# Kernel optimization log

Measured on AMD Instinct MI355X. Metric: run time of the kernel, lower is better.

## Reference

```python
import jax, jax.numpy as jnp
import numpy as np

B, S, D, H = 4, 2048, 1024, 16
HD = D // H
THETA = 10000.0


def rope(x, pos, theta=THETA):
    # x: [..., seq, d], pos: broadcastable to [..., seq]
    d = x.shape[-1]
    half = d // 2
    inv_freq = 1.0 / (theta ** (jnp.arange(half, dtype=jnp.float32) * 2.0 / d))  # [half]
    ang = pos[..., None].astype(jnp.float32) * inv_freq  # [..., seq, half]
    cos, sin = jnp.cos(ang), jnp.sin(ang)
    x1, x2 = x[..., 0::2], x[..., 1::2]
    r1 = x1 * cos - x2 * sin
    r2 = x1 * sin + x2 * cos
    return jnp.stack([r1, r2], axis=-1).reshape(x.shape).astype(x.dtype)


def setup_inputs() -> dict:
    key = jax.random.key(0)
    ks = jax.random.split(key, 5)
    x = jax.random.normal(ks[0], (B, S, D), dtype=jnp.float32)
    token_positions = jnp.tile(jnp.arange(S, dtype=jnp.int64 if jax.config.jax_enable_x64 else jnp.int32), (B, 1))
    scale = 0.02
    Wq = jax.random.normal(ks[1], (D, D), dtype=jnp.float32) * scale
    Wk = jax.random.normal(ks[2], (D, D), dtype=jnp.float32) * scale
    Wv = jax.random.normal(ks[3], (D, D), dtype=jnp.float32) * scale
    Wo = jax.random.normal(ks[4], (D, D), dtype=jnp.float32) * scale
    return {"x": x, "token_positions": token_positions, "Wq": Wq, "Wk": Wk, "Wv": Wv, "Wo": Wo}


def reference(x, token_positions, Wq, Wk, Wv, Wo):
    b, s, d = x.shape
    # QKV projections (torch Linear: x @ W.T), split heads -> [b, h, s, hd]
    def proj(W):
        y = jnp.einsum('bsd,ed->bse', x, W)
        return y.reshape(b, s, H, HD).transpose(0, 2, 1, 3)
    Q, K, V = proj(Wq), proj(Wk), proj(Wv)
    # token_positions [..., seq] -> [..., 1, seq] to broadcast over heads
    pos = token_positions[:, None, :]  # [b, 1, s]
    Q = rope(Q, pos)
    K = rope(K, pos)
    # causal mask and scaled dot-product attention
    idx = jnp.arange(s)
    causal = idx[:, None] >= idx[None, :]  # [s, s], query >= key
    scores = jnp.einsum('bhqd,bhkd->bhqk', Q, K) / jnp.sqrt(jnp.float32(HD))
    scores = jnp.where(causal, scores, -jnp.inf)
    weights = jax.nn.softmax(scores, axis=-1)
    o = jnp.einsum('bhqk,bhkd->bhqd', weights, V)
    o = o.transpose(0, 2, 1, 3).reshape(b, s, d)  # merge heads
    return jnp.einsum('bsd,ed->bse', o, Wo)
```

## Files before the change

### kernel.cpp

```cpp
#include <hip/hip_runtime.h>

#define S_LEN 2048
#define NH 16
#define HDIM 64
#define DMODEL 1024

typedef __attribute__((ext_vector_type(8))) short bf16x8;
typedef __attribute__((ext_vector_type(4))) float f32x4;

__device__ __forceinline__ short f2bf(float f) {
    union { float f; unsigned u; } x; x.f = f;
    unsigned r = x.u + 0x7fffu + ((x.u >> 16) & 1u);
    return (short)(r >> 16);
}

#define GLDS(g, l) __builtin_amdgcn_global_load_lds( \
    (__attribute__((address_space(1))) void*)(g),    \
    (__attribute__((address_space(3))) void*)(l), 16, 0, 0)

#define QSCALE 0.18033688011112042f
#define FREQ_L 0.41524101186109327f

__global__ __launch_bounds__(256) void prep(const float* __restrict__ x,
                                            const float* __restrict__ wq,
                                            const float* __restrict__ wk,
                                            const float* __restrict__ wv,
                                            const float* __restrict__ wo,
                                            const int* __restrict__ tp,
                                            short* __restrict__ xb,
                                            short* __restrict__ wqb,
                                            short* __restrict__ wkb,
                                            short* __restrict__ wvb,
                                            short* __restrict__ wob,
                                            float2* __restrict__ tab) {
    int bid = blockIdx.x;
    if (bid < 8192) {
        int i = bid * 256 + threadIdx.x;
        float4 v = ((const float4*)x)[i];
        short4 o;
        o.x = f2bf(v.x); o.y = f2bf(v.y); o.z = f2bf(v.z); o.w = f2bf(v.w);
        ((short4*)xb)[i] = o;
    } else if (bid < 12288) {
        int sel = (bid - 8192) >> 10;
        const float* in = sel == 0 ? wq : sel == 1 ? wk : sel == 2 ? wv : wo;
        short* out = sel == 0 ? wqb : sel == 1 ? wkb : sel == 2 ? wvb : wob;
        int i = ((bid - 8192) & 1023) * 256 + threadIdx.x;
        float4 v = ((const float4*)in)[i];
        short4 o;
        o.x = f2bf(v.x); o.y = f2bf(v.y); o.z = f2bf(v.z); o.w = f2bf(v.w);
        ((short4*)out)[i] = o;
    } else {
        int idx = (bid - 12288) * 256 + threadIdx.x;
        int b = idx >> 16, s = (idx >> 5) & 2047, i = idx & 31;
        float p = (float)tp[(b << 11) + s];
        float freq = exp2f(-(float)i * FREQ_L);
        float sn, cs;
        sincosf(p * freq, &sn, &cs);
        tab[idx] = make_float2(cs, sn);
    }
}

__global__ __launch_bounds__(512) void gemm_qkv(const short* __restrict__ A,
                                                const short* __restrict__ Bq,
                                                const short* __restrict__ Bk,
                                                const short* __restrict__ Bv,
                                                const float2* __restrict__ tab,
                                                short* __restrict__ Qo,
                                                short* __restrict__ Ko,
                                                short* __restrict__ Vo) {
    constexpr int K = 1024;
    __shared__ __align__(16) short smem[3 * 24576];

    const int sel = blockIdx.x >> 3;
    const int bn = blockIdx.x & 7;
    const int bm = blockIdx.y;
    const short* Bm = sel == 0 ? Bq : sel == 1 ? Bk : Bv;
    short* Cb = sel == 0 ? Qo : sel == 1 ? Ko : Vo;

    const int tid = threadIdx.x;
    const int lane = tid & 63;
    const int w = tid >> 6;
    const int wm = w >> 1;
    const int wn = w & 1;
    const int quad = lane >> 4, l16 = lane & 15;
    const int l7 = l16 & 7;

    int aoff[4], boff[2];
#pragma unroll
    for (int i = 0; i < 4; i++) {
        int Lc = i * 512 + tid;
        int row = Lc >> 3;
        int cc = (Lc & 7) ^ (row & 7);
        aoff[i] = (bm * 256 + row) * K + cc * 8;
    }
#pragma unroll
    for (int i = 0; i < 2; i++) {
        int Lc = i * 512 + tid;
        int row = Lc >> 3;
        int cc = (Lc & 7) ^ (row & 7);
        boff[i] = (bn * 128 + row) * K + cc * 8;
    }

    auto stage = [&](int h, int slot) {
        char* sbase = (char*)smem + slot * 49152;
        const int kh = h * 64;
#pragma unroll
        for (int i = 0; i < 4; i++)
            GLDS(A + aoff[i] + kh, sbase + i * 8192 + w * 1024);
#pragma unroll
        for (int i = 0; i < 2; i++)
            GLDS(Bm + boff[i] + kh, sbase + 32768 + i * 8192 + w * 1024);
    };

    f32x4 acc[4][4] = {};

    auto compute = [&](int slot) {
        const short* sA = smem + slot * 24576;
        const short* sB = sA + 16384;
#pragma unroll
        for (int kc = 0; kc < 2; kc++) {
            const int c = ((kc * 4 + quad) ^ l7) * 8;
            bf16x8 af[4], bfm[4];
#pragma unroll
            for (int mi = 0; mi < 4; mi++)
                af[mi] = *(const bf16x8*)&sA[(wm * 64 + mi * 16 + l16) * 64 + c];
#pragma unroll
            for (int ni = 0; ni < 4; ni++)
                bfm[ni] = *(const bf16x8*)&sB[(wn * 64 + ni * 16 + l16) * 64 + c];
            __builtin_amdgcn_s_setprio(1);
#pragma unroll
            for (int mi = 0; mi < 4; mi++)
#pragma unroll
                for (int ni = 0; ni < 4; ni++)
                    acc[mi][ni] = __builtin_amdgcn_mfma_f32_16x16x32_bf16(af[mi], bfm[ni],
                                                                          acc[mi][ni], 0, 0, 0);
            __builtin_amdgcn_s_setprio(0);
        }
    };

    stage(0, 0); stage(1, 1);

    auto step = [&](int h, int sc, int ss) {
        asm volatile("s_waitcnt vmcnt(6)" ::: "memory");
        __builtin_amdgcn_s_barrier();
        __builtin_amdgcn_sched_barrier(0);
        stage(h + 2, ss);
        compute(sc);
    };

    for (int h = 0; h < 12; h += 3) {
        step(h + 0, 0, 2);
        step(h + 1, 1, 0);
        step(h + 2, 2, 1);
    }
    step(12, 0, 2);
    step(13, 1, 0);
    asm volatile("s_waitcnt vmcnt(6)" ::: "memory");
    __builtin_amdgcn_s_barrier();
    __builtin_amdgcn_sched_barrier(0);
    compute(2);
    asm volatile("s_waitcnt vmcnt(0)" ::: "memory");
    __builtin_amdgcn_s_barrier();
    __builtin_amdgcn_sched_barrier(0);
    compute(0);

    const int gm0 = bm * 256 + wm * 64;
    const int gn0 = bn * 128 + wn * 64;

    if (sel == 2) {
        short* T = smem;
        __syncthreads();
#pragma unroll
        for (int mi = 0; mi < 4; mi++) {
            int lmb = wm * 64 + mi * 16 + quad * 4;
#pragma unroll
            for (int ni = 0; ni < 4; ni++) {
                int ln = wn * 64 + ni * 16 + l16;
                short4 pk;
                pk.x = f2bf(acc[mi][ni][0]);
                pk.y = f2bf(acc[mi][ni][1]);
                pk.z = f2bf(acc[mi][ni][2]);
                pk.w = f2bf(acc[mi][ni][3]);
                *(short4*)&T[ln * 256 + (lmb ^ ((ln & 31) << 3))] = pk;
            }
        }
        __syncthreads();
        const int row = tid >> 2, qt = tid & 3;
        const int grow = bn * 128 + row;
        const int gb = bm >> 3;
        const int gs0 = (bm & 7) * 256;
        short* dst = Cb + (((size_t)(gb * NH + (grow >> 6)) * HDIM + (grow & 63)) * S_LEN
                           + gs0 + qt * 64);
#pragma unroll
        for (int j = 0; j < 8; j++) {
            bf16x8 v = *(const bf16x8*)&T[row * 256 +
                        ((qt * 64 + j * 8) ^ ((row & 31) << 3))];
            *(bf16x8*)(dst + j * 8) = v;
        }
    } else {
        const float qs = (sel == 0) ? QSCALE : 1.0f;
#pragma unroll
        for (int mi = 0; mi < 4; mi++)
#pragma unroll
            for (int r = 0; r < 4; r++) {
                int gm = gm0 + mi * 16 + quad * 4 + r;
                const float2* trow = tab + (gm << 5);
                int b = gm >> 11, s = gm & 2047;
#pragma unroll
                for (int ni = 0; ni < 4; ni++) {
                    float2 cs = trow[ni * 8 + (l16 >> 1)];
                    float v = acc[mi][ni][r];
                    float prt = __shfl_xor(v, 1, 64);
                    float val = (l16 & 1) ? (prt * cs.y + v * cs.x)
                                          : (v * cs.x - prt * cs.y);
                    int gn = gn0 + ni * 16 + l16;
                    int h = gn >> 6, hd = gn & 63;
                    Cb[((b * NH + h) * S_LEN + s) * HDIM + hd] = f2bf(val * qs);
                }
            }
    }
}

__global__ __launch_bounds__(256) void gemm_o(const short* __restrict__ A,
                                              const short* __restrict__ Bw,
                                              float* __restrict__ Cf) {
    constexpr int N = 1024, K = 1024, BK = 32;
    __shared__ __align__(16) short sa[3][128 * BK];
    __shared__ __align__(16) short sb[3][64 * BK];

    const int tid = threadIdx.x;
    const int lane = tid & 63;
    const int w = tid >> 6;
    const int quad = lane >> 4, l16 = lane & 15;
    const int bn = blockIdx.x, bm = blockIdx.y;
    const int arow0 = bm * 128, brow0 = bn * 64;

    int aoff[2], boff;
#pragma unroll
    for (int i = 0; i < 2; i++) {
        int cs = i * 256 + tid;
        int row = cs >> 2;
        int gc = (cs & 3) ^ ((row >> 1) & 3);
        aoff[i] = (arow0 + row) * K + gc * 8;
    }
    {
        int row = tid >> 2;
        int gc = (tid & 3) ^ ((row >> 1) & 3);
        boff = (brow0 + row) * K + gc * 8;
    }

    auto stage = [&](int kt, int b) {
        const int k0 = kt * BK;
#pragma unroll
        for (int i = 0; i < 2; i++)
            GLDS(A + aoff[i] + k0, (char*)&sa[b][0] + i * 4096 + w * 1024);
        GLDS(Bw + boff + k0, (char*)&sb[b][0] + w * 1024);
    };

    f32x4 acc[2][4] = {};
    const int rsw = (quad ^ ((l16 >> 1) & 3)) * 8;

    auto compute = [&](int b) {
        bf16x8 af[2];
#pragma unroll
        for (int mi = 0; mi < 2; mi++)
            af[mi] = *(const bf16x8*)&sa[b][(w * 32 + mi * 16 + l16) * BK + rsw];
#pragma unroll
        for (int ni = 0; ni < 4; ni++) {
            bf16x8 bfr = *(const bf16x8*)&sb[b][(ni * 16 + l16) * BK + rsw];
#pragma unroll
            for (int mi = 0; mi < 2; mi++)
                acc[mi][ni] = __builtin_amdgcn_mfma_f32_16x16x32_bf16(af[mi], bfr,
                                                                     acc[mi][ni], 0, 0, 0);
        }
    };

    stage(0, 0);
    stage(1, 1);

    auto step = [&](int kt, int b, int bs) {
        asm volatile("s_waitcnt vmcnt(3)" ::: "memory");
        __builtin_amdgcn_s_barrier();
        __builtin_amdgcn_sched_barrier(0);
        stage(kt + 2, bs);
        compute(b);
    };

    for (int kt = 0; kt < 30; kt += 3) {
        step(kt + 0, 0, 2);
        step(kt + 1, 1, 0);
        step(kt + 2, 2, 1);
    }
    asm volatile("s_waitcnt vmcnt(3)" ::: "memory");
    __builtin_amdgcn_s_barrier();
    __builtin_amdgcn_sched_barrier(0);
    compute(0);
    asm volatile("s_waitcnt vmcnt(0)" ::: "memory");
    __builtin_amdgcn_s_barrier();
    __builtin_amdgcn_sched_barrier(0);
    compute(1);

    const int gm0 = arow0 + w * 32;
#pragma unroll
    for (int mi = 0; mi < 2; mi++)
#pragma unroll
        for (int ni = 0; ni < 4; ni++)
#pragma unroll
            for (int r = 0; r < 4; r++) {
                int gm = gm0 + mi * 16 + quad * 4 + r;
                int gn = brow0 + ni * 16 + l16;
                Cf[gm * N + gn] = acc[mi][ni][r];
            }
}

__global__ __launch_bounds__(256, 2) void attn(const short* __restrict__ Q,
                                               const short* __restrict__ Km,
                                               const short* __restrict__ Vt,
                                               short* __restrict__ O) {
    __shared__ __align__(16) short kbuf[3][64 * 64];
    __shared__ __align__(16) short vbuf[3][64 * 64];
    __shared__ __align__(16) short pbuf[4][32 * 64];

    const int lane = threadIdx.x & 63;
    const int w = threadIdx.x >> 6;
    const int quad = lane >> 4, l16 = lane & 15;
    const int l7 = l16 & 7;
    const int bh = blockIdx.y;

    const short* Qg = Q  + bh * S_LEN * 64;
    const short* Kg = Km + bh * S_LEN * 64;
    const short* Vg = Vt + bh * 64 * S_LEN;
    short* myp = &pbuf[w][0];

    const int b = bh >> 4, h = bh & 15;

    bf16x8 ones;
#pragma unroll
    for (int j = 0; j < 8; j++) ones[j] = (short)0x3f80;

    auto stage = [&](int kt, int slot) {
        const short* kt_base = Kg + kt * 64 * 64;
        const short* vt_base = Vg + kt * 64;
#pragma unroll
        for (int i = 0; i < 2; ++i) {
            int ch = w * 128 + i * 64 + lane;
            int row = ch >> 3;
            int c = (ch & 7) ^ (row & 7);
            GLDS(kt_base + row * 64 + c * 8, (char*)&kbuf[slot][(w * 128 + i * 64) * 8]);
        }
#pragma unroll
        for (int i = 0; i < 2; ++i) {
            int ch = w * 128 + i * 64 + lane;
            int row = ch >> 3;
            int c = (ch & 7) ^ (row & 7);
            GLDS(vt_base + row * S_LEN + c * 8, (char*)&vbuf[slot][(w * 128 + i * 64) * 8]);
        }
    };

    const int QtA = blockIdx.x;
    const int QtB = 15 - blockIdx.x;

    bf16x8 apA[2][2], apB[2][2];
    int s0 = 0;
    stage(0, 0);

    for (int phase = 0; phase < 2; ++phase) {
        const int Qt = phase ? QtB : QtA;
        const int nkt = 2 * Qt + 2;

        bf16x8 aq[2][2];
#pragma unroll
        for (int mi = 0; mi < 2; mi++) {
            int qrow = Qt * 128 + w * 32 + mi * 16 + l16;
#pragma unroll
            for (int kc = 0; kc < 2; kc++)
                aq[mi][kc] = *(const bf16x8*)&Qg[qrow * 64 + kc * 32 + quad * 8];
        }

        f32x4 oacc[2][4] = {};
        f32x4 lacc[2] = {};

        auto iter = [&](int kt, int scur, int snext, int sprev,
                        bf16x8 (&apc)[2][2], bf16x8 (&app)[2][2], bool hasPrev) {
            __syncthreads();
            int stk = kt + 1;
            if (stk < nkt)       stage(stk, snext);
            else if (phase == 0) stage(0,   snext);
            const short* kb = &kbuf[scur][0];
            const short* vb = &vbuf[sprev][0];

            f32x4 sc[2][4] = {};
            __builtin_amdgcn_s_setprio(1);
#pragma unroll
            for (int nt = 0; nt < 4; nt++) {
                int raddr = (nt * 16 + l16) * 64;
#pragma unroll
                for (int kc = 0; kc < 2; kc++) {
                    bf16x8 kf = *(const bf16x8*)&kb[raddr + (((quad + kc * 4) ^ l7) * 8)];
                    sc[0][nt] = __builtin_amdgcn_mfma_f32_16x16x32_bf16(aq[0][kc], kf, sc[0][nt], 0, 0, 0);
                    sc[1][nt] = __builtin_amdgcn_mfma_f32_16x16x32_bf16(aq[1][kc], kf, sc[1][nt], 0, 0, 0);
                }
            }
            if (hasPrev) {
#pragma unroll
                for (int nt = 0; nt < 4; nt++) {
                    int raddr = (nt * 16 + l16) * 64;
#pragma unroll
                    for (int kc = 0; kc < 2; kc++) {
                        bf16x8 vf = *(const bf16x8*)&vb[raddr + (((quad + kc * 4) ^ l7) * 8)];
                        oacc[0][nt] = __builtin_amdgcn_mfma_f32_16x16x32_bf16(app[0][kc], vf, oacc[0][nt], 0, 0, 0);
                        oacc[1][nt] = __builtin_amdgcn_mfma_f32_16x16x32_bf16(app[1][kc], vf, oacc[1][nt], 0, 0, 0);
                    }
                }
#pragma unroll
                for (int mi = 0; mi < 2; mi++) {
                    lacc[mi] = __builtin_amdgcn_mfma_f32_16x16x32_bf16(app[mi][0], ones, lacc[mi], 0, 0, 0);
                    lacc[mi] = __builtin_amdgcn_mfma_f32_16x16x32_bf16(app[mi][1], ones, lacc[mi], 0, 0, 0);
                }
            }
            __builtin_amdgcn_s_setprio(0);

            if (kt >= nkt - 2) {
#pragma unroll
                for (int mi = 0; mi < 2; mi++)
#pragma unroll
                    for (int nt = 0; nt < 4; nt++)
#pragma unroll
                        for (int r = 0; r < 4; r++) {
                            int col = kt * 64 + nt * 16 + l16;
                            int row = Qt * 128 + w * 32 + mi * 16 + quad * 4 + r;
                            if (col > row) sc[mi][nt][r] = -__builtin_inff();
                        }
            }
#pragma unroll
            for (int mi = 0; mi < 2; mi++)
#pragma unroll
                for (int nt = 0; nt < 4; nt++)
#pragma unroll
                    for (int r = 0; r < 4; r++) {
                        float pv = __builtin_amdgcn_exp2f(sc[mi][nt][r]);
                        int q = mi * 16 + quad * 4 + r;
                        union { float f; unsigned short us[2]; } uu;
                        uu.f = pv;
                        myp[q * 64 + (((nt * 2 + (l16 >> 3)) ^ (q & 7)) * 8) + l7] =
                            (short)uu.us[1];
                    }
#pragma unroll
            for (int mi = 0; mi < 2; mi++)
#pragma unroll
                for (int kc = 0; kc < 2; kc++)
                    apc[mi][kc] = *(const bf16x8*)&myp[(mi * 16 + l16) * 64 +
                                                       (((quad + kc * 4) ^ l7) * 8)];
        };

        for (int kt = 0; kt < nkt; kt += 2) {
            int s1 = s0 + 1; if (s1 == 3) s1 = 0;
            int s2 = s1 + 1; if (s2 == 3) s2 = 0;
            iter(kt,     s0, s1, s2, apA, apB, kt > 0);
            iter(kt + 1, s1, s2, s0, apB, apA, true);
            s0 = s2;
        }
        {
            int slast = s0 - 1; if (slast < 0) slast = 2;
            const short* vb = &vbuf[slast][0];
            __builtin_amdgcn_s_setprio(1);
#pragma unroll
            for (int nt = 0; nt < 4; nt++) {
                int raddr = (nt * 16 + l16) * 64;
#pragma unroll
                for (int kc = 0; kc < 2; kc++) {
                    bf16x8 vf = *(const bf16x8*)&vb[raddr + (((quad + kc * 4) ^ l7) * 8)];
                    oacc[0][nt] = __builtin_amdgcn_mfma_f32_16x16x32_bf16(apB[0][kc], vf, oacc[0][nt], 0, 0, 0);
                    oacc[1][nt] = __builtin_amdgcn_mfma_f32_16x16x32_bf16(apB[1][kc], vf, oacc[1][nt], 0, 0, 0);
                }
            }
#pragma unroll
            for (int mi = 0; mi < 2; mi++) {
                lacc[mi] = __builtin_amdgcn_mfma_f32_16x16x32_bf16(apB[mi][0], ones, lacc[mi], 0, 0, 0);
                lacc[mi] = __builtin_amdgcn_mfma_f32_16x16x32_bf16(apB[mi][1], ones, lacc[mi], 0, 0, 0);
            }
            __builtin_amdgcn_s_setprio(0);
        }
#pragma unroll
        for (int mi = 0; mi < 2; mi++)
#pragma unroll
            for (int r = 0; r < 4; r++) {
                float inv = 1.0f / lacc[mi][r];
                int srow = Qt * 128 + w * 32 + mi * 16 + quad * 4 + r;
#pragma unroll
                for (int nt = 0; nt < 4; nt++) {
                    int hd = nt * 16 + l16;
                    O[(b * S_LEN + srow) * DMODEL + h * HDIM + hd] = f2bf(oacc[mi][nt][r] * inv);
                }
            }
    }
}

extern "C" void kernel_launch(void* const* d_in, const int* in_sizes, int n_in,
                              void* d_out, int out_size, void* d_ws, size_t ws_size,
                              hipStream_t stream) {
    const float* x  = (const float*)d_in[0];
    const int*   tp = (const int*)d_in[1];
    const float* Wq = (const float*)d_in[2];
    const float* Wk = (const float*)d_in[3];
    const float* Wv = (const float*)d_in[4];
    const float* Wo = (const float*)d_in[5];
    float* out = (float*)d_out;

    char* ws = (char*)d_ws;
    const size_t MB = 1024 * 1024;
    short* xb  = (short*)(ws);
    short* wqb = (short*)(ws + 16 * MB);
    short* wkb = (short*)(ws + 18 * MB);
    short* wvb = (short*)(ws + 20 * MB);
    short* wob = (short*)(ws + 22 * MB);
    short* Qb  = (short*)(ws + 24 * MB);
    short* Kb  = (short*)(ws + 40 * MB);
    short* Vtb = (short*)(ws + 56 * MB);
    float2* tab = (float2*)d_out;

    prep<<<13312, 256, 0, stream>>>(x, Wq, Wk, Wv, Wo, tp,
                                    xb, wqb, wkb, wvb, wob, tab);

    gemm_qkv<<<dim3(24, 32), 512, 0, stream>>>(xb, wqb, wkb, wvb, tab, Qb, Kb, Vtb);

    attn<<<dim3(8, 64), 256, 0, stream>>>(Qb, Kb, Vtb, xb);

    gemm_o<<<dim3(16, 64), 256, 0, stream>>>(xb, wob, out);
}
```

Baseline: 245.4 us.

## Retile output projection GEMM to 256x128 blocks and reorder grid dimensions

The output projection GEMM moves from 128x64 tiles with BK=32 and 256 threads to 256x128 tiles with BK=64, 512 threads and a 4x4 MFMA accumulator per wave, matching the QKV GEMM structure. This raises arithmetic intensity per LDS load and cuts redundant global reads of A and B. All three main kernels also swap grid x/y so that consecutive workgroups share the same B or head tile, which should improve L2 reuse and dispatch order. The bigger tile gives only 256 workgroups, which could underfill the GPU's CUs and adds register pressure.

```diff
diff --git a/kernel.cpp b/kernel.cpp
--- a/kernel.cpp
+++ b/kernel.cpp
@@ -71,9 +71,9 @@
     constexpr int K = 1024;
     __shared__ __align__(16) short smem[3 * 24576];
 
-    const int sel = blockIdx.x >> 3;
-    const int bn = blockIdx.x & 7;
-    const int bm = blockIdx.y;
+    const int bm = blockIdx.x;
+    const int sel = blockIdx.y >> 3;
+    const int bn = blockIdx.y & 7;
     const short* Bm = sel == 0 ? Bq : sel == 1 ? Bk : Bv;
     short* Cb = sel == 0 ? Qo : sel == 1 ? Ko : Vo;
 
@@ -221,94 +221,112 @@
     }
 }
 
-__global__ __launch_bounds__(256) void gemm_o(const short* __restrict__ A,
+__global__ __launch_bounds__(512) void gemm_o(const short* __restrict__ A,
                                               const short* __restrict__ Bw,
                                               float* __restrict__ Cf) {
-    constexpr int N = 1024, K = 1024, BK = 32;
-    __shared__ __align__(16) short sa[3][128 * BK];
-    __shared__ __align__(16) short sb[3][64 * BK];
+    constexpr int K = 1024, N = 1024;
+    __shared__ __align__(16) short smem[3 * 24576];
+
+    const int bm = blockIdx.x;
+    const int bn = blockIdx.y;
 
     const int tid = threadIdx.x;
     const int lane = tid & 63;
     const int w = tid >> 6;
+    const int wm = w >> 1;
+    const int wn = w & 1;
     const int quad = lane >> 4, l16 = lane & 15;
-    const int bn = blockIdx.x, bm = blockIdx.y;
-    const int arow0 = bm * 128, brow0 = bn * 64;
-
-    int aoff[2], boff;
+    const int l7 = l16 & 7;
+
+    int aoff[4], boff[2];
+#pragma unroll
+    for (int i = 0; i < 4; i++) {
+        int Lc = i * 512 + tid;
+        int row = Lc >> 3;
+        int cc = (Lc & 7) ^ (row & 7);
+        aoff[i] = (bm * 256 + row) * K + cc * 8;
+    }
 #pragma unroll
     for (int i = 0; i < 2; i++) {
-        int cs = i * 256 + tid;
-        int row = cs >> 2;
-        int gc = (cs & 3) ^ ((row >> 1) & 3);
-        aoff[i] = (arow0 + row) * K + gc * 8;
-    }
-    {
-        int row = tid >> 2;
-        int gc = (tid & 3) ^ ((row >> 1) & 3);
-        boff = (brow0 + row) * K + gc * 8;
-    }
-
-    auto stage = [&](int kt, int b) {
-        const int k0 = kt * BK;
+        int Lc = i * 512 + tid;
+        int row = Lc >> 3;
+        int cc = (Lc & 7) ^ (row & 7);
+        boff[i] = (bn * 128 + row) * K + cc * 8;
+    }
+
+    auto stage = [&](int h, int slot) {
+        char* sbase = (char*)smem + slot * 49152;
+        const int kh = h * 64;
+#pragma unroll
+        for (int i = 0; i < 4; i++)
+            GLDS(A + aoff[i] + kh, sbase + i * 8192 + w * 1024);
 #pragma unroll
         for (int i = 0; i < 2; i++)
-            GLDS(A + aoff[i] + k0, (char*)&sa[b][0] + i * 4096 + w * 1024);
-        GLDS(Bw + boff + k0, (char*)&sb[b][0] + w * 1024);
-    };
-
-    f32x4 acc[2][4] = {};
-    const int rsw = (quad ^ ((l16 >> 1) & 3)) * 8;
-
-    auto compute = [&](int b) {
-        bf16x8 af[2];
-#pragma unroll
-        for (int mi = 0; mi < 2; mi++)
-            af[mi] = *(const bf16x8*)&sa[b][(w * 32 + mi * 16 + l16) * BK + rsw];
-#pragma unroll
-        for (int ni = 0; ni < 4; ni++) {
-            bf16x8 bfr = *(const bf16x8*)&sb[b][(ni * 16 + l16) * BK + rsw];
-#pragma unroll
-            for (int mi = 0; mi < 2; mi++)
-                acc[mi][ni] = __builtin_amdgcn_mfma_f32_16x16x32_bf16(af[mi], bfr,
-                                                                     acc[mi][ni], 0, 0, 0);
-        }
-    };
-
-    stage(0, 0);
-    stage(1, 1);
-
-    auto step = [&](int kt, int b, int bs) {
-        asm volatile("s_waitcnt vmcnt(3)" ::: "memory");
+            GLDS(Bw + boff[i] + kh, sbase + 32768 + i * 8192 + w * 1024);
+    };
+
+    f32x4 acc[4][4] = {};
+
+    auto compute = [&](int slot) {
+        const short* sA = smem + slot * 24576;
+        const short* sB = sA + 16384;
+#pragma unroll
+        for (int kc = 0; kc < 2; kc++) {
+            const int c = ((kc * 4 + quad) ^ l7) * 8;
+            bf16x8 af[4], bfm[4];
+#pragma unroll
+            for (int mi = 0; mi < 4; mi++)
+                af[mi] = *(const bf16x8*)&sA[(wm * 64 + mi * 16 + l16) * 64 + c];
+#pragma unroll
+            for (int ni = 0; ni < 4; ni++)
+                bfm[ni] = *(const bf16x8*)&sB[(wn * 64 + ni * 16 + l16) * 64 + c];
+            __builtin_amdgcn_s_setprio(1);
+#pragma unroll
+            for (int mi = 0; mi < 4; mi++)
+#pragma unroll
+                for (int ni = 0; ni < 4; ni++)
+                    acc[mi][ni] = __builtin_amdgcn_mfma_f32_16x16x32_bf16(af[mi], bfm[ni],
+                                                                          acc[mi][ni], 0, 0, 0);
+            __builtin_amdgcn_s_setprio(0);
+        }
+    };
+
+    stage(0, 0); stage(1, 1);
+
+    auto step = [&](int h, int sc, int ss) {
+        asm volatile("s_waitcnt vmcnt(6)" ::: "memory");
         __builtin_amdgcn_s_barrier();
         __builtin_amdgcn_sched_barrier(0);
-        stage(kt + 2, bs);
-        compute(b);
-    };
-
-    for (int kt = 0; kt < 30; kt += 3) {
-        step(kt + 0, 0, 2);
-        step(kt + 1, 1, 0);
-        step(kt + 2, 2, 1);
-    }
-    asm volatile("s_waitcnt vmcnt(3)" ::: "memory");
+        stage(h + 2, ss);
+        compute(sc);
+    };
+
+    for (int h = 0; h < 12; h += 3) {
+        step(h + 0, 0, 2);
+        step(h + 1, 1, 0);
+        step(h + 2, 2, 1);
+    }
+    step(12, 0, 2);
+    step(13, 1, 0);
+    asm volatile("s_waitcnt vmcnt(6)" ::: "memory");
+    __builtin_amdgcn_s_barrier();
+    __builtin_amdgcn_sched_barrier(0);
+    compute(2);
+    asm volatile("s_waitcnt vmcnt(0)" ::: "memory");
     __builtin_amdgcn_s_barrier();
     __builtin_amdgcn_sched_barrier(0);
     compute(0);
-    asm volatile("s_waitcnt vmcnt(0)" ::: "memory");
-    __builtin_amdgcn_s_barrier();
-    __builtin_amdgcn_sched_barrier(0);
-    compute(1);
-
-    const int gm0 = arow0 + w * 32;
-#pragma unroll
-    for (int mi = 0; mi < 2; mi++)
+
+    const int gm0 = bm * 256 + wm * 64;
+    const int gn0 = bn * 128 + wn * 64;
+#pragma unroll
+    for (int mi = 0; mi < 4; mi++)
 #pragma unroll
         for (int ni = 0; ni < 4; ni++)
 #pragma unroll
             for (int r = 0; r < 4; r++) {
                 int gm = gm0 + mi * 16 + quad * 4 + r;
-                int gn = brow0 + ni * 16 + l16;
+                int gn = gn0 + ni * 16 + l16;
                 Cf[gm * N + gn] = acc[mi][ni][r];
             }
 }
@@ -325,7 +343,7 @@
     const int w = threadIdx.x >> 6;
     const int quad = lane >> 4, l16 = lane & 15;
     const int l7 = l16 & 7;
-    const int bh = blockIdx.y;
+    const int bh = blockIdx.x;
 
     const short* Qg = Q  + bh * S_LEN * 64;
     const short* Kg = Km + bh * S_LEN * 64;
@@ -357,8 +375,8 @@
         }
     };
 
-    const int QtA = blockIdx.x;
-    const int QtB = 15 - blockIdx.x;
+    const int QtA = blockIdx.y;
+    const int QtB = 15 - blockIdx.y;
 
     bf16x8 apA[2][2], apB[2][2];
     int s0 = 0;
@@ -522,9 +540,9 @@
     prep<<<13312, 256, 0, stream>>>(x, Wq, Wk, Wv, Wo, tp,
                                     xb, wqb, wkb, wvb, wob, tab);
 
-    gemm_qkv<<<dim3(24, 32), 512, 0, stream>>>(xb, wqb, wkb, wvb, tab, Qb, Kb, Vtb);
-
-    attn<<<dim3(8, 64), 256, 0, stream>>>(Qb, Kb, Vtb, xb);
-
-    gemm_o<<<dim3(16, 64), 256, 0, stream>>>(xb, wob, out);
+    gemm_qkv<<<dim3(32, 24), 512, 0, stream>>>(xb, wqb, wkb, wvb, tab, Qb, Kb, Vtb);
+
+    attn<<<dim3(64, 8), 256, 0, stream>>>(Qb, Kb, Vtb, xb);
+
+    gemm_o<<<dim3(32, 8), 512, 0, stream>>>(xb, wob, out);
 }
```

Result: faster. 228.1 us (-7.0%).
